# Optimization experiments

Hardware: AMD Instinct MI355X
Metric: run time of the kernel (lower is better)

The kernel has to match this reference:

```python
import jax, jax.numpy as jnp
import numpy as np
from jax import lax

B, S, T = 32, 24, 48           # batch, max_num_strokes, max_stroke_len
ENC, SCH, STH = 512, 512, 512  # enc_dim, scene_hdim, stroke_hdim


def _w(k, shape):
    return (jax.random.normal(k, shape, jnp.float32) / np.sqrt(shape[-1])).astype(jnp.float32)


def setup_inputs() -> dict:
    key = jax.random.key(0)
    ks = jax.random.split(key, 12)
    return {
        "enc_features": jax.random.normal(ks[0], (B, ENC), jnp.float32),
        "vector_sketch": jax.random.normal(ks[1], (B, S, T, 5), jnp.float32),
        # force max length == T and num strokes == S so torch's dynamic .max()
        # bounds coincide with the static shapes used here
        "batch_num_strokes": jnp.full((B, 1), S, jnp.int32),
        "batch_stroke_len": jax.random.randint(ks[2], (B, S), 1, T + 1, jnp.int32).at[0, 0].set(T),
        # scene LSTMCell (input = enc_dim + stroke_hdim), torch gate order i,f,g,o
        "W_sc_ih": _w(ks[3], (4 * SCH, ENC + STH)),
        "W_sc_hh": _w(ks[4], (4 * SCH, SCH)),
        "b_sc": jnp.zeros((4 * SCH,), jnp.float32),  # b_ih + b_hh folded
        # stroke LSTM layer 0 (input = scene_hdim + 5)
        "W0_ih": _w(ks[5], (4 * STH, SCH + 5)),
        "W0_hh": _w(ks[6], (4 * STH, STH)),
        "b0": jnp.zeros((4 * STH,), jnp.float32),
        # stroke LSTM layer 1 (input = stroke_hdim)
        "W1_ih": _w(ks[7], (4 * STH, STH)),
        "W1_hh": _w(ks[8], (4 * STH, STH)),
        "b1": jnp.zeros((4 * STH,), jnp.float32),
        # linear_output: stroke_hdim -> 5
        "W_out": _w(ks[9], (5, STH)),
        "b_out": jnp.zeros((5,), jnp.float32),
    }


def _lstm_cell(x, h, c, Wih, Whh, b):
    g = x @ Wih.T + h @ Whh.T + b
    i, f, gg, o = jnp.split(g, 4, axis=-1)
    c = jax.nn.sigmoid(f) * c + jax.nn.sigmoid(i) * jnp.tanh(gg)
    return jax.nn.sigmoid(o) * jnp.tanh(c), c


def _forward(enc_features, vector_sketch, W_sc_ih, W_sc_hh, b_sc, W0_ih, W0_hh, b0,
             W1_ih, W1_hh, b1, W_out, b_out, batch_stroke_len):
    nb = enc_features.shape[0]
    zs = jnp.zeros((nb, SCH), jnp.float32)
    init_tok0 = jnp.tile(jnp.array([[0., 0., 1., 0., 0.]], jnp.float32), (nb, 1))
    t_idx = jnp.arange(T + 1)

    def stroke_step(carry, xs):
        scene_h, scene_c, prev_tok, init_tok = carry
        sketch_s, lens_s = xs                       # (B,T,5), (B,)
        ctx = jnp.concatenate([enc_features, prev_tok], axis=-1)
        scene_h2, scene_c2 = _lstm_cell(ctx, scene_h, scene_c, W_sc_ih, W_sc_hh, b_sc)
        coords = jnp.concatenate([init_tok[:, None, :], sketch_s], axis=1)  # (B,T+1,5)
        lengths = lens_s + 1                        # pack lengths

        def time_step(c2, xt):
            h0, c0, h1, c1 = c2
            x_t, t = xt
            m = (t < lengths)[:, None]              # packed-sequence validity mask
            h0n, c0n = _lstm_cell(jnp.concatenate([scene_h2, x_t], axis=-1), h0, c0, W0_ih, W0_hh, b0)
            h1n, c1n = _lstm_cell(h0n, h1, c1, W1_ih, W1_hh, b1)
            h0 = jnp.where(m, h0n, h0); c0 = jnp.where(m, c0n, c0)
            h1 = jnp.where(m, h1n, h1); c1 = jnp.where(m, c1n, c1)
            return (h0, c0, h1, c1), jnp.where(m, h1, 0.0)  # pad_packed zero-pads outputs

        z = jnp.zeros((nb, STH), jnp.float32)
        (_, _, h1f, _), outs = lax.scan(time_step, (z, z, z, z), (jnp.swapaxes(coords, 0, 1), t_idx))
        # linear applied AFTER zero-padding, so padded-but-within-L steps get the bias (matches torch)
        out_coords = jnp.swapaxes(outs, 0, 1) @ W_out.T + b_out      # (B,T+1,5)
        L = jnp.max(lens_s)
        valid = (jnp.arange(T) < L)[None, :, None]
        stroke_out = jnp.where(valid, out_coords[:, :T, :], 0.0)     # (B,T,5)
        prev_tok = lax.stop_gradient(h1f)          # .detach() in torch
        last = jnp.clip(lens_s - 1, 0, None)
        init_tok2 = jnp.take_along_axis(sketch_s, last[:, None, None], axis=1)[:, 0, :]
        return (scene_h2, scene_c2, prev_tok, init_tok2), stroke_out

    xs = (jnp.swapaxes(vector_sketch, 0, 1), batch_stroke_len.T)     # (S,B,T,5), (S,B)
    _, outs = lax.scan(stroke_step, (zs, zs, zs, init_tok0), xs)
    return jnp.transpose(outs, (1, 0, 2, 3))       # (B,S,T,5)


def reference(enc_features, vector_sketch, batch_num_strokes, batch_stroke_len,
              W_sc_ih, W_sc_hh, b_sc, W0_ih, W0_hh, b0, W1_ih, W1_hh, b1, W_out, b_out):
    # batch_num_strokes only sets the (static) stroke loop bound S
    del batch_num_strokes
    return _forward(enc_features, vector_sketch, W_sc_ih, W_sc_hh, b_sc, W0_ih, W0_hh,
                    b0, W1_ih, W1_hh, b1, W_out, b_out, batch_stroke_len)
```

## Files before the change

kernel.cpp:

```cpp
#include <hip/hip_runtime.h>

#define NB 256
#define NT 256
#define AGT __HIP_MEMORY_SCOPE_AGENT
typedef unsigned long long ull;
typedef _Float16 f16;
typedef __attribute__((ext_vector_type(8))) _Float16 f16x8;
typedef __attribute__((ext_vector_type(4))) float f32x4;


#define BSTR 1056

struct __align__(16) SMem {
  unsigned short Bt[2][2][4 * 528];
  float X[2][4][8];
  int sLens[2][4];
  int sLmax[2];
};

__device__ __forceinline__ float sigm(float x) { return 1.0f / (1.0f + expf(-x)); }
__device__ __forceinline__ unsigned short f16b(float x) {
  union { _Float16 h; unsigned short u; } q; q.h = (_Float16)x; return q.u;
}
__device__ __forceinline__ ull pk4(float a, float b, float c, float d) {
  union { _Float16 h; unsigned short u; } q;
  ull r; q.h = (_Float16)a; r = q.u; q.h = (_Float16)b; r |= (ull)q.u << 16;
  q.h = (_Float16)c; r |= (ull)q.u << 32; q.h = (_Float16)d; r |= (ull)q.u << 48;
  return r;
}
__device__ __forceinline__ ull lda8(const ull* p) {
  return __hip_atomic_load(p, __ATOMIC_RELAXED, AGT);
}

extern "C" __global__ void __launch_bounds__(NT, 1)
rnn_decoder_kernel(const float* __restrict__ enc, const float* __restrict__ sketch,
                   const int* __restrict__ slen,
                   const float* __restrict__ Wsc_ih, const float* __restrict__ Wsc_hh,
                   const float* __restrict__ bsc,
                   const float* __restrict__ W0ih, const float* __restrict__ W0hh,
                   const float* __restrict__ b0,
                   const float* __restrict__ W1ih, const float* __restrict__ W1hh,
                   const float* __restrict__ b1,
                   const float* __restrict__ Wout, const float* __restrict__ bout,
                   float* __restrict__ out, float* __restrict__ ws)
{
  extern __shared__ char smraw[];
  SMem* sm = (SMem*)smraw;
  const int tid = threadIdx.x;
  const int w = blockIdx.x;
  const int team = w >> 5, slot = w & 31;
  const int lane = tid & 63;
  const int wq = tid >> 6;
  const int l15 = lane & 15;
  const int kq = lane >> 4;
  const int my_b = l15 & 3;
  const int my_u = wq * 4 + kq;

  ull* tb = (ull*)ws + (size_t)team * 6144;
  ull* h0T = tb;
  ull* h1T = tb + 2048;
  ull* sHg = tb + 4096;

  auto grow = [&](int r) { return ((r & 3) << 9) + slot * 16 + (r >> 2); };

  auto ldsB = [&](const unsigned short* Bp, int st) -> f16x8 {
    return *(const f16x8*)((const char*)Bp + my_b * BSTR + st * 64 + kq * 16);
  };
  auto mfma_gv = [&](const float* W, int stride, int coloff, const unsigned short* Bp, f32x4& acc) {
    const float* rp = W + (size_t)grow(wq * 16 + l15) * stride + coloff;
#pragma unroll
    for (int st = 0; st < 16; ++st) {
      const float* q = rp + st * 32 + kq * 8;
      float4 u0 = *(const float4*)q, u1 = *(const float4*)(q + 4);
      f16x8 a;
      a[0] = (f16)u0.x; a[1] = (f16)u0.y; a[2] = (f16)u0.z; a[3] = (f16)u0.w;
      a[4] = (f16)u1.x; a[5] = (f16)u1.y; a[6] = (f16)u1.z; a[7] = (f16)u1.w;
      acc = __builtin_amdgcn_mfma_f32_16x16x32_f16(a, ldsB(Bp, st), acc, 0, 0, 0);
    }
  };
  auto mfma_gs = [&](const float* W, const unsigned short* Bp, f32x4& acc) {
    const float* rp = W + (size_t)grow(wq * 16 + l15) * 517;
#pragma unroll
    for (int st = 0; st < 16; ++st) {
      const float* q = rp + st * 32 + kq * 8;
      f16x8 a;
#pragma unroll
      for (int j = 0; j < 8; ++j) a[j] = (f16)q[j];
      acc = __builtin_amdgcn_mfma_f32_16x16x32_f16(a, ldsB(Bp, st), acc, 0, 0, 0);
    }
  };

  auto stage4 = [&](const ull* s0, unsigned e0, unsigned short* Bp) {
    const ull* pA = s0 + 2 * tid;
    const ull* pB = pA + 1;
    const ull* pC = s0 + 512 + 2 * tid;
    const ull* pD = pC + 1;
    ull a = lda8(pA), b = lda8(pB), c = lda8(pC), d = lda8(pD);
    int spins = 0;
    while ((((unsigned)(a >> 32) ^ e0) | ((unsigned)(b >> 32) ^ e0) |
            ((unsigned)(c >> 32) ^ e0) | ((unsigned)(d >> 32) ^ e0)) != 0) {
      if (++spins > 40000) break;
      if (spins > 16) __builtin_amdgcn_s_sleep(1);
      if ((unsigned)(a >> 32) != e0) a = lda8(pA);
      if ((unsigned)(b >> 32) != e0) b = lda8(pB);
      if ((unsigned)(c >> 32) != e0) c = lda8(pC);
      if ((unsigned)(d >> 32) != e0) d = lda8(pD);
    }
    {
      int bb2 = tid >> 7, up = (2 * tid) & 255;
      *(ull*)((char*)Bp + bb2 * BSTR + up * 4) =
          (ull)(unsigned)a | ((ull)(unsigned)b << 32);
      int t2 = tid + 256;
      int bb3 = t2 >> 7, up2 = (2 * t2) & 255;
      *(ull*)((char*)Bp + bb3 * BSTR + up2 * 4) =
          (ull)(unsigned)c | ((ull)(unsigned)d << 32);
    }
  };

  f16x8 w0hh[16], w1ih[16], whh[16];
  {
    const float* r0 = W0hh + (size_t)grow(wq * 16 + l15) * 512;
    const float* r1 = W1ih + (size_t)grow(wq * 16 + l15) * 512;
    const float* r2 = W1hh + (size_t)grow(wq * 16 + l15) * 512;
#pragma unroll
    for (int st = 0; st < 16; ++st) {
      const int o = st * 32 + kq * 8;
      float4 u0, u1;
      f16x8 a;
      u0 = *(const float4*)(r0 + o); u1 = *(const float4*)(r0 + o + 4);
      a[0] = (f16)u0.x; a[1] = (f16)u0.y; a[2] = (f16)u0.z; a[3] = (f16)u0.w;
      a[4] = (f16)u1.x; a[5] = (f16)u1.y; a[6] = (f16)u1.z; a[7] = (f16)u1.w;
      w0hh[st] = a;
      u0 = *(const float4*)(r1 + o); u1 = *(const float4*)(r1 + o + 4);
      a[0] = (f16)u0.x; a[1] = (f16)u0.y; a[2] = (f16)u0.z; a[3] = (f16)u0.w;
      a[4] = (f16)u1.x; a[5] = (f16)u1.y; a[6] = (f16)u1.z; a[7] = (f16)u1.w;
      w1ih[st] = a;
      u0 = *(const float4*)(r2 + o); u1 = *(const float4*)(r2 + o + 4);
      a[0] = (f16)u0.x; a[1] = (f16)u0.y; a[2] = (f16)u0.z; a[3] = (f16)u0.w;
      a[4] = (f16)u1.x; a[5] = (f16)u1.y; a[6] = (f16)u1.z; a[7] = (f16)u1.w;
      whh[st] = a;
    }
  }
  float cb0[4], cb1[4], cbsc[4], cwx[4][5];
  {
    int gu = slot * 16 + my_u;
#pragma unroll
    for (int gi = 0; gi < 4; ++gi) {
      int gr = gi * 512 + gu;
      cb0[gi] = b0[gr]; cb1[gi] = b1[gr]; cbsc[gi] = bsc[gr];
#pragma unroll
      for (int j = 0; j < 5; ++j) cwx[gi][j] = W0ih[(size_t)gr * 517 + 512 + j];
    }
  }
  const int b_o = slot / 5, o_o = slot % 5;
  const bool oslot = (slot < 20);
  float wo[8]; float bo_r = 0.f;
  if (oslot && tid < 64) {
    bo_r = bout[o_o];
#pragma unroll
    for (int j = 0; j < 8; ++j) wo[j] = Wout[o_o * 512 + lane * 8 + j];
  }

  f32x4 e0reg = {0.f, 0.f, 0.f, 0.f};
  {
    int b2 = tid >> 6, c8 = tid & 63;
    const float* q = enc + (size_t)(4 * team + b2) * 512 + c8 * 8;
    float4 u0 = *(const float4*)q, u1 = *(const float4*)(q + 4);
    unsigned short* Bp = &sm->Bt[0][0][0];
    *(ull*)((char*)Bp + b2 * BSTR + c8 * 16) = pk4(u0.x, u0.y, u0.z, u0.w);
    *(ull*)((char*)Bp + b2 * BSTR + c8 * 16 + 8) = pk4(u1.x, u1.y, u1.z, u1.w);
    __syncthreads();
    mfma_gv(Wsc_ih, 1024, 0, Bp, e0reg);
  }

  float o_csc = 0.f, o_c0 = 0.f, o_h0 = 0.f, o_c1 = 0.f, o_h1 = 0.f;
  int pp = 0;

  for (int s = 0; s < 24; ++s) {
    const unsigned base = 51u * (unsigned)s;

    pp ^= 1;
    {
      int lv = (tid < 32) ? slen[tid * 24 + s] : 0;
      if (tid < 64) {
#pragma unroll
        for (int o2 = 1; o2 < 64; o2 <<= 1) lv = max(lv, __shfl_xor(lv, o2, 64));
        if (tid == 0) sm->sLmax[s & 1] = lv;
      }
      if (tid < 4) sm->sLens[s & 1][tid] = slen[(4 * team + tid) * 24 + s];
    }
    {
      unsigned short* Bp0 = &sm->Bt[pp][0][0];
      unsigned short* Bp1 = &sm->Bt[pp][1][0];
      if (s > 0) {
        stage4(h1T, base, Bp0);
        stage4(sHg + ((s - 1) & 1) * 1024, base - 50u, Bp1);
      }
      __syncthreads();
      f32x4 asc = {0.f, 0.f, 0.f, 0.f};
      if (s > 0) {
        mfma_gv(Wsc_ih, 1024, 512, Bp0, asc);
        mfma_gv(Wsc_hh, 512, 0, Bp1, asc);
      }
      float g[4];
#pragma unroll
      for (int gi = 0; gi < 4; ++gi) g[gi] = e0reg[gi] + cbsc[gi] + asc[gi];
      float c = sigm(g[1]) * o_csc + sigm(g[0]) * tanhf(g[2]);
      float h = sigm(g[3]) * tanhf(c);
      o_csc = c;
      o_c0 = o_h0 = o_c1 = o_h1 = 0.f;
      float hhi = __shfl_down(h, 16, 64);
      if (((kq & 1) == 0) && (l15 < 4)) {
        int chunk = my_b * 256 + slot * 8 + wq * 2 + (kq >> 1);
        unsigned pay = (unsigned)f16b(h) | ((unsigned)f16b(hhi) << 16);
        __hip_atomic_store(&sHg[(s & 1) * 1024 + chunk],
                           (ull)pay | ((ull)(base + 1u) << 32), __ATOMIC_RELAXED, AGT);
      }
    }

    pp ^= 1;
    f32x4 s0reg = {0.f, 0.f, 0.f, 0.f};
    {
      unsigned short* Bp0 = &sm->Bt[pp][0][0];
      if (tid < 4) {
        float xv[5];
        if (s == 0) { xv[0] = 0.f; xv[1] = 0.f; xv[2] = 1.f; xv[3] = 0.f; xv[4] = 0.f; }
        else {
          int bgl = 4 * team + tid;
          int lp = slen[bgl * 24 + (s - 1)];
          int last = min(max(lp - 1, 0), 47);
          const float* q = sketch + ((bgl * 24 + (s - 1)) * 48 + last) * 5;
#pragma unroll
          for (int j = 0; j < 5; ++j) xv[j] = q[j];
        }
#pragma unroll
        for (int j = 0; j < 5; ++j) sm->X[pp][tid][j] = xv[j];
      }
      stage4(sHg + (s & 1) * 1024, base + 1u, Bp0);
      __syncthreads();
      mfma_gs(W0ih, Bp0, s0reg);
      float g[4];
#pragma unroll
      for (int gi = 0; gi < 4; ++gi) {
        float xd = 0.f;
#pragma unroll
        for (int j = 0; j < 5; ++j) xd += cwx[gi][j] * sm->X[pp][my_b][j];
        g[gi] = s0reg[gi] + cb0[gi] + xd;
      }
      float c = sigm(g[1]) * o_c0 + sigm(g[0]) * tanhf(g[2]);
      o_c0 = c; o_h0 = sigm(g[3]) * tanhf(c);
      float hhi = __shfl_down(o_h0, 16, 64);
      if (((kq & 1) == 0) && (l15 < 4)) {
        int chunk = my_b * 256 + slot * 8 + wq * 2 + (kq >> 1);
        unsigned pay = (unsigned)f16b(o_h0) | ((unsigned)f16b(hhi) << 16);
        __hip_atomic_store(&h0T[chunk],
                           (ull)pay | ((ull)(base + 2u) << 32), __ATOMIC_RELAXED, AGT);
      }
    }

    for (int k = 0; k <= 48; ++k) {
      const bool doL0 = (k < 48), doPrev = (k > 0);
      const unsigned eSeq = base + 2u + (unsigned)k, sSeq = eSeq + 1u;
      pp ^= 1;
      unsigned short* B0p = &sm->Bt[pp][0][0];
      unsigned short* B1p = &sm->Bt[pp][1][0];
      if (doL0 && tid < 4) {
        const float* q = sketch + (((4 * team + tid) * 24 + s) * 48 + k) * 5;
#pragma unroll
        for (int j = 0; j < 5; ++j) sm->X[pp][tid][j] = q[j];
      }
      stage4(h0T + (k & 1) * 1024, eSeq, B0p);
      __syncthreads();

      f32x4 a0 = {0.f, 0.f, 0.f, 0.f}, a1 = {0.f, 0.f, 0.f, 0.f};
#pragma unroll
      for (int st = 0; st < 16; ++st) {
        f16x8 bb = ldsB(B0p, st);
        if (doL0) a0 = __builtin_amdgcn_mfma_f32_16x16x32_f16(w0hh[st], bb, a0, 0, 0, 0);
        a1 = __builtin_amdgcn_mfma_f32_16x16x32_f16(w1ih[st], bb, a1, 0, 0, 0);
      }
      const int Lb = sm->sLens[s & 1][my_b];
      if (doL0) {
        if ((k + 1) <= Lb) {
          float g[4];
#pragma unroll
          for (int gi = 0; gi < 4; ++gi) {
            float xd = 0.f;
#pragma unroll
            for (int j = 0; j < 5; ++j) xd += cwx[gi][j] * sm->X[pp][my_b][j];
            g[gi] = a0[gi] + s0reg[gi] + cb0[gi] + xd;
          }
          float c = sigm(g[1]) * o_c0 + sigm(g[0]) * tanhf(g[2]);
          o_c0 = c; o_h0 = sigm(g[3]) * tanhf(c);
        }
        float hhi0 = __shfl_down(o_h0, 16, 64);
        if (((kq & 1) == 0) && (l15 < 4)) {
          int chunk = my_b * 256 + slot * 8 + wq * 2 + (kq >> 1);
          unsigned p0 = (unsigned)f16b(o_h0) | ((unsigned)f16b(hhi0) << 16);
          __hip_atomic_store(&h0T[((k + 1) & 1) * 1024 + chunk],
                             (ull)p0 | ((ull)sSeq << 32), __ATOMIC_RELAXED, AGT);
        }
      }
      if (doPrev) {
        stage4(h1T + ((k - 1) & 1) * 1024, eSeq, B1p);
        __syncthreads();
#pragma unroll
        for (int st = 0; st < 16; ++st)
          a1 = __builtin_amdgcn_mfma_f32_16x16x32_f16(whh[st], ldsB(B1p, st), a1, 0, 0, 0);
      }
      if (k <= Lb) {
        float g[4];
#pragma unroll
        for (int gi = 0; gi < 4; ++gi) g[gi] = a1[gi] + cb1[gi];
        float c = sigm(g[1]) * o_c1 + sigm(g[0]) * tanhf(g[2]);
        o_c1 = c; o_h1 = sigm(g[3]) * tanhf(c);
      }
      float hhi1 = __shfl_down(o_h1, 16, 64);
      if (((kq & 1) == 0) && (l15 < 4)) {
        int chunk = my_b * 256 + slot * 8 + wq * 2 + (kq >> 1);
        unsigned p1 = (unsigned)f16b(o_h1) | ((unsigned)f16b(hhi1) << 16);
        __hip_atomic_store(&h1T[(k & 1) * 1024 + chunk],
                           (ull)p1 | ((ull)sSeq << 32), __ATOMIC_RELAXED, AGT);
      }

      if (doPrev && oslot && tid < 64) {
        f16x8 hv = *(const f16x8*)((const char*)B1p + b_o * BSTR + lane * 16);
        float sd = 0.f;
#pragma unroll
        for (int j = 0; j < 8; ++j) sd += (float)hv[j] * wo[j];
#pragma unroll
        for (int o2 = 1; o2 < 64; o2 <<= 1) sd += __shfl_xor(sd, o2, 64);
        if (tid == 0) {
          int tt = k - 1;
          float val = 0.f;
          if (tt < sm->sLmax[s & 1])
            val = (tt > sm->sLens[s & 1][b_o]) ? bo_r : (sd + bo_r);
          out[(((4 * team + b_o) * 24 + s) * 48 + tt) * 5 + o_o] = val;
        }
      }
    }
  }
}

extern "C" void kernel_launch(void* const* d_in, const int* in_sizes, int n_in,
                              void* d_out, int out_size, void* d_ws, size_t ws_size,
                              hipStream_t stream) {
  (void)in_sizes; (void)n_in; (void)out_size; (void)ws_size;
  int lds_bytes = 98304;
  hipFuncSetAttribute((const void*)rnn_decoder_kernel,
                      hipFuncAttributeMaxDynamicSharedMemorySize, lds_bytes);
  hipMemsetAsync(d_ws, 0, 8 * 6144 * 8, stream);
  rnn_decoder_kernel<<<dim3(NB), dim3(NT), lds_bytes, stream>>>(
      (const float*)d_in[0],
      (const float*)d_in[1],
      (const int*)d_in[3],
      (const float*)d_in[4],
      (const float*)d_in[5],
      (const float*)d_in[6],
      (const float*)d_in[7],
      (const float*)d_in[8],
      (const float*)d_in[9],
      (const float*)d_in[10],
      (const float*)d_in[11],
      (const float*)d_in[12],
      (const float*)d_in[13],
      (const float*)d_in[14],
      (float*)d_out, (float*)d_ws);
}
```

Before: 4.057 ms.

## Stage recurrent hidden states per-wave to remove block barriers in time loop

Inside the 48-step inner recurrence, each wave now polls and stages the full h0/h1 vectors into its own private LDS buffer, using batched inline-asm cache-bypassing loads. This removes the two __syncthreads per step. The stroke's sketch inputs are preloaded into LDS once per stroke instead of once per step, and the output projection is spread across waves. The cost is redundant global polling traffic, four times the LDS staging work, and reliance on inline asm with sc0 sc1 for coherent reads.

```diff
diff --git a/kernel.cpp b/kernel.cpp
--- a/kernel.cpp
+++ b/kernel.cpp
@@ -7,13 +7,16 @@
 typedef _Float16 f16;
 typedef __attribute__((ext_vector_type(8))) _Float16 f16x8;
 typedef __attribute__((ext_vector_type(4))) float f32x4;
+typedef __attribute__((ext_vector_type(4))) unsigned u32x4;
 
 
 #define BSTR 1056
 
 struct __align__(16) SMem {
-  unsigned short Bt[2][2][4 * 528];
-  float X[2][4][8];
+  unsigned short Wv[4][2][4 * 528];
+  unsigned short Bs[2][4 * 528];
+  float Xs[48][4][8];
+  float X0[4][8];
   int sLens[2][4];
   int sLmax[2];
 };
@@ -30,6 +33,22 @@
 }
 __device__ __forceinline__ ull lda8(const ull* p) {
   return __hip_atomic_load(p, __ATOMIC_RELAXED, AGT);
+}
+__device__ __forceinline__ u32x4 ld1x16(const void* p) {
+  u32x4 r;
+  asm volatile("global_load_dwordx4 %0, %1, off sc0 sc1\ns_waitcnt vmcnt(0)"
+               : "=&v"(r) : "v"(p) : "memory");
+  return r;
+}
+__device__ __forceinline__ void issue4(const void* p0, const void* p1,
+                                       const void* p2, const void* p3,
+                                       u32x4& a, u32x4& b, u32x4& c, u32x4& d) {
+  asm volatile("global_load_dwordx4 %0, %4, off sc0 sc1\n"
+               "global_load_dwordx4 %1, %5, off sc0 sc1\n"
+               "global_load_dwordx4 %2, %6, off sc0 sc1\n"
+               "global_load_dwordx4 %3, %7, off sc0 sc1"
+               : "=&v"(a), "=&v"(b), "=&v"(c), "=&v"(d)
+               : "v"(p0), "v"(p1), "v"(p2), "v"(p3) : "memory");
 }
 
 extern "C" __global__ void __launch_bounds__(NT, 1)
@@ -117,6 +136,43 @@
     }
   };
 
+  auto stageW = [&](const ull* s0, unsigned e0, unsigned short* Wt) {
+    const char* p = (const char*)(s0 + 16 * lane);
+    u32x4 v0, v1, v2, v3, v4, v5, v6, v7;
+    issue4(p, p + 16, p + 32, p + 48, v0, v1, v2, v3);
+    issue4(p + 64, p + 80, p + 96, p + 112, v4, v5, v6, v7);
+    asm volatile("s_waitcnt vmcnt(0)"
+                 : "+v"(v0), "+v"(v1), "+v"(v2), "+v"(v3),
+                   "+v"(v4), "+v"(v5), "+v"(v6), "+v"(v7) :: "memory");
+    int spins = 0;
+    for (;;) {
+      unsigned bad = (v0.y ^ e0) | (v0.w ^ e0) | (v1.y ^ e0) | (v1.w ^ e0) |
+                     (v2.y ^ e0) | (v2.w ^ e0) | (v3.y ^ e0) | (v3.w ^ e0) |
+                     (v4.y ^ e0) | (v4.w ^ e0) | (v5.y ^ e0) | (v5.w ^ e0) |
+                     (v6.y ^ e0) | (v6.w ^ e0) | (v7.y ^ e0) | (v7.w ^ e0);
+      if (!bad) break;
+      if (++spins > 40000) break;
+      if (spins > 16) __builtin_amdgcn_s_sleep(1);
+      if ((v0.y ^ e0) | (v0.w ^ e0)) v0 = ld1x16(p);
+      if ((v1.y ^ e0) | (v1.w ^ e0)) v1 = ld1x16(p + 16);
+      if ((v2.y ^ e0) | (v2.w ^ e0)) v2 = ld1x16(p + 32);
+      if ((v3.y ^ e0) | (v3.w ^ e0)) v3 = ld1x16(p + 48);
+      if ((v4.y ^ e0) | (v4.w ^ e0)) v4 = ld1x16(p + 64);
+      if ((v5.y ^ e0) | (v5.w ^ e0)) v5 = ld1x16(p + 80);
+      if ((v6.y ^ e0) | (v6.w ^ e0)) v6 = ld1x16(p + 96);
+      if ((v7.y ^ e0) | (v7.w ^ e0)) v7 = ld1x16(p + 112);
+    }
+    char* d = (char*)Wt + (lane >> 4) * BSTR + 64 * l15;
+    *(ull*)(d)      = (ull)v0.x | ((ull)v0.z << 32);
+    *(ull*)(d + 8)  = (ull)v1.x | ((ull)v1.z << 32);
+    *(ull*)(d + 16) = (ull)v2.x | ((ull)v2.z << 32);
+    *(ull*)(d + 24) = (ull)v3.x | ((ull)v3.z << 32);
+    *(ull*)(d + 32) = (ull)v4.x | ((ull)v4.z << 32);
+    *(ull*)(d + 40) = (ull)v5.x | ((ull)v5.z << 32);
+    *(ull*)(d + 48) = (ull)v6.x | ((ull)v6.z << 32);
+    *(ull*)(d + 56) = (ull)v7.x | ((ull)v7.z << 32);
+  };
+
   f16x8 w0hh[16], w1ih[16], whh[16];
   {
     const float* r0 = W0hh + (size_t)grow(wq * 16 + l15) * 512;
@@ -154,8 +210,9 @@
   }
   const int b_o = slot / 5, o_o = slot % 5;
   const bool oslot = (slot < 20);
+  const int owave = slot & 3;
   float wo[8]; float bo_r = 0.f;
-  if (oslot && tid < 64) {
+  if (oslot) {
     bo_r = bout[o_o];
 #pragma unroll
     for (int j = 0; j < 8; ++j) wo[j] = Wout[o_o * 512 + lane * 8 + j];
@@ -166,7 +223,7 @@
     int b2 = tid >> 6, c8 = tid & 63;
     const float* q = enc + (size_t)(4 * team + b2) * 512 + c8 * 8;
     float4 u0 = *(const float4*)q, u1 = *(const float4*)(q + 4);
-    unsigned short* Bp = &sm->Bt[0][0][0];
+    unsigned short* Bp = &sm->Bs[0][0];
     *(ull*)((char*)Bp + b2 * BSTR + c8 * 16) = pk4(u0.x, u0.y, u0.z, u0.w);
     *(ull*)((char*)Bp + b2 * BSTR + c8 * 16 + 8) = pk4(u1.x, u1.y, u1.z, u1.w);
     __syncthreads();
@@ -174,12 +231,12 @@
   }
 
   float o_csc = 0.f, o_c0 = 0.f, o_h0 = 0.f, o_c1 = 0.f, o_h1 = 0.f;
-  int pp = 0;
+  unsigned short* myB0 = &sm->Wv[wq][0][0];
+  unsigned short* myB1 = &sm->Wv[wq][1][0];
 
   for (int s = 0; s < 24; ++s) {
     const unsigned base = 51u * (unsigned)s;
 
-    pp ^= 1;
     {
       int lv = (tid < 32) ? slen[tid * 24 + s] : 0;
       if (tid < 64) {
@@ -190,8 +247,8 @@
       if (tid < 4) sm->sLens[s & 1][tid] = slen[(4 * team + tid) * 24 + s];
     }
     {
-      unsigned short* Bp0 = &sm->Bt[pp][0][0];
-      unsigned short* Bp1 = &sm->Bt[pp][1][0];
+      unsigned short* Bp0 = &sm->Bs[0][0];
+      unsigned short* Bp1 = &sm->Bs[1][0];
       if (s > 0) {
         stage4(h1T, base, Bp0);
         stage4(sHg + ((s - 1) & 1) * 1024, base - 50u, Bp1);
@@ -218,10 +275,10 @@
       }
     }
 
-    pp ^= 1;
     f32x4 s0reg = {0.f, 0.f, 0.f, 0.f};
     {
-      unsigned short* Bp0 = &sm->Bt[pp][0][0];
+      __syncthreads();
+      unsigned short* Bp0 = &sm->Bs[0][0];
       if (tid < 4) {
         float xv[5];
         if (s == 0) { xv[0] = 0.f; xv[1] = 0.f; xv[2] = 1.f; xv[3] = 0.f; xv[4] = 0.f; }
@@ -234,7 +291,12 @@
           for (int j = 0; j < 5; ++j) xv[j] = q[j];
         }
 #pragma unroll
-        for (int j = 0; j < 5; ++j) sm->X[pp][tid][j] = xv[j];
+        for (int j = 0; j < 5; ++j) sm->X0[tid][j] = xv[j];
+      }
+      for (int e = tid; e < 960; e += NT) {
+        int k2 = e / 20, r2 = e % 20, b2 = r2 / 5, j2 = r2 % 5;
+        sm->Xs[k2][b2][j2] =
+            sketch[(((4 * team + b2) * 24 + s) * 48 + k2) * 5 + j2];
       }
       stage4(sHg + (s & 1) * 1024, base + 1u, Bp0);
       __syncthreads();
@@ -244,7 +306,7 @@
       for (int gi = 0; gi < 4; ++gi) {
         float xd = 0.f;
 #pragma unroll
-        for (int j = 0; j < 5; ++j) xd += cwx[gi][j] * sm->X[pp][my_b][j];
+        for (int j = 0; j < 5; ++j) xd += cwx[gi][j] * sm->X0[my_b][j];
         g[gi] = s0reg[gi] + cb0[gi] + xd;
       }
       float c = sigm(g[1]) * o_c0 + sigm(g[0]) * tanhf(g[2]);
@@ -258,36 +320,27 @@
       }
     }
 
+    const int Lb = sm->sLens[s & 1][my_b];
+    const int Lmax_s = sm->sLmax[s & 1];
+    const int Lb_o = sm->sLens[s & 1][oslot ? b_o : 0];
+
     for (int k = 0; k <= 48; ++k) {
       const bool doL0 = (k < 48), doPrev = (k > 0);
       const unsigned eSeq = base + 2u + (unsigned)k, sSeq = eSeq + 1u;
-      pp ^= 1;
-      unsigned short* B0p = &sm->Bt[pp][0][0];
-      unsigned short* B1p = &sm->Bt[pp][1][0];
-      if (doL0 && tid < 4) {
-        const float* q = sketch + (((4 * team + tid) * 24 + s) * 48 + k) * 5;
-#pragma unroll
-        for (int j = 0; j < 5; ++j) sm->X[pp][tid][j] = q[j];
-      }
-      stage4(h0T + (k & 1) * 1024, eSeq, B0p);
-      __syncthreads();
-
+
+      stageW(h0T + (k & 1) * 1024, eSeq, myB0);
       f32x4 a0 = {0.f, 0.f, 0.f, 0.f}, a1 = {0.f, 0.f, 0.f, 0.f};
-#pragma unroll
-      for (int st = 0; st < 16; ++st) {
-        f16x8 bb = ldsB(B0p, st);
-        if (doL0) a0 = __builtin_amdgcn_mfma_f32_16x16x32_f16(w0hh[st], bb, a0, 0, 0, 0);
-        a1 = __builtin_amdgcn_mfma_f32_16x16x32_f16(w1ih[st], bb, a1, 0, 0, 0);
-      }
-      const int Lb = sm->sLens[s & 1][my_b];
       if (doL0) {
+#pragma unroll
+        for (int st = 0; st < 16; ++st)
+          a0 = __builtin_amdgcn_mfma_f32_16x16x32_f16(w0hh[st], ldsB(myB0, st), a0, 0, 0, 0);
         if ((k + 1) <= Lb) {
           float g[4];
 #pragma unroll
           for (int gi = 0; gi < 4; ++gi) {
             float xd = 0.f;
 #pragma unroll
-            for (int j = 0; j < 5; ++j) xd += cwx[gi][j] * sm->X[pp][my_b][j];
+            for (int j = 0; j < 5; ++j) xd += cwx[gi][j] * sm->Xs[k][my_b][j];
             g[gi] = a0[gi] + s0reg[gi] + cb0[gi] + xd;
           }
           float c = sigm(g[1]) * o_c0 + sigm(g[0]) * tanhf(g[2]);
@@ -300,13 +353,17 @@
           __hip_atomic_store(&h0T[((k + 1) & 1) * 1024 + chunk],
                              (ull)p0 | ((ull)sSeq << 32), __ATOMIC_RELAXED, AGT);
         }
-      }
+        asm volatile("" ::: "memory");
+      }
+#pragma unroll
+      for (int st = 0; st < 16; ++st)
+        a1 = __builtin_amdgcn_mfma_f32_16x16x32_f16(w1ih[st], ldsB(myB0, st), a1, 0, 0, 0);
+
       if (doPrev) {
-        stage4(h1T + ((k - 1) & 1) * 1024, eSeq, B1p);
-        __syncthreads();
+        stageW(h1T + ((k - 1) & 1) * 1024, eSeq, myB1);
 #pragma unroll
         for (int st = 0; st < 16; ++st)
-          a1 = __builtin_amdgcn_mfma_f32_16x16x32_f16(whh[st], ldsB(B1p, st), a1, 0, 0, 0);
+          a1 = __builtin_amdgcn_mfma_f32_16x16x32_f16(whh[st], ldsB(myB1, st), a1, 0, 0, 0);
       }
       if (k <= Lb) {
         float g[4];
@@ -322,19 +379,19 @@
         __hip_atomic_store(&h1T[(k & 1) * 1024 + chunk],
                            (ull)p1 | ((ull)sSeq << 32), __ATOMIC_RELAXED, AGT);
       }
-
-      if (doPrev && oslot && tid < 64) {
-        f16x8 hv = *(const f16x8*)((const char*)B1p + b_o * BSTR + lane * 16);
+      asm volatile("" ::: "memory");
+
+      if (doPrev && oslot && wq == owave) {
+        f16x8 hv = *(const f16x8*)((const char*)myB1 + b_o * BSTR + lane * 16);
         float sd = 0.f;
 #pragma unroll
         for (int j = 0; j < 8; ++j) sd += (float)hv[j] * wo[j];
 #pragma unroll
         for (int o2 = 1; o2 < 64; o2 <<= 1) sd += __shfl_xor(sd, o2, 64);
-        if (tid == 0) {
+        if (lane == 0) {
           int tt = k - 1;
           float val = 0.f;
-          if (tt < sm->sLmax[s & 1])
-            val = (tt > sm->sLens[s & 1][b_o]) ? bo_r : (sd + bo_r);
+          if (tt < Lmax_s) val = (tt > Lb_o) ? bo_r : (sd + bo_r);
           out[(((4 * team + b_o) * 24 + s) * 48 + tt) * 5 + o_o] = val;
         }
       }
```

After: 8.125 ms. 100% more time.

## Split block waves into layer-0 and layer-1 groups with LDS flag handoff

Applied to the files above, without the earlier changes.

Each block's four waves are specialised: two waves run the layer-0 stroke LSTM recurrence and two run layer 1, each wave handling two gate tiles, instead of all waves doing both layers in lockstep. Workgroup-scoped LDS flags replace __syncthreads inside the time loop so layer 0 can run ahead on step k+1 while layer 1 finishes step k. h0 gets a 4-deep ring buffer and the per-stroke sketch inputs are preloaded into LDS. Register pressure rises from holding 32-fragment weight arrays per wave, and the flag-based spin synchronisation is more fragile than barriers.

```diff
diff --git a/kernel.cpp b/kernel.cpp
--- a/kernel.cpp
+++ b/kernel.cpp
@@ -3,6 +3,7 @@
 #define NB 256
 #define NT 256
 #define AGT __HIP_MEMORY_SCOPE_AGENT
+#define WGS __HIP_MEMORY_SCOPE_WORKGROUP
 typedef unsigned long long ull;
 typedef _Float16 f16;
 typedef __attribute__((ext_vector_type(8))) _Float16 f16x8;
@@ -12,10 +13,17 @@
 #define BSTR 1056
 
 struct __align__(16) SMem {
-  unsigned short Bt[2][2][4 * 528];
-  float X[2][4][8];
+  unsigned short T0[2][4 * 528];
+  unsigned short T1[2][4 * 528];
+  unsigned short Bs[2][4 * 528];
+  float Xs[48][4][8];
+  float X0[4][8];
+  float sS0[16][4][4];
+  float sC0[16][4];
+  float sH0[16][4];
   int sLens[2][4];
   int sLmax[2];
+  unsigned gFlag[8];
 };
 
 __device__ __forceinline__ float sigm(float x) { return 1.0f / (1.0f + expf(-x)); }
@@ -55,28 +63,31 @@
   const int kq = lane >> 4;
   const int my_b = l15 & 3;
   const int my_u = wq * 4 + kq;
-
-  ull* tb = (ull*)ws + (size_t)team * 6144;
+  const int wid2 = wq & 1;
+  const int uA = 8 * wid2 + kq, uB = uA + 4;
+
+  ull* tb = (ull*)ws + (size_t)team * 8192;
   ull* h0T = tb;
-  ull* h1T = tb + 2048;
-  ull* sHg = tb + 4096;
+  ull* h1T = tb + 4096;
+  ull* sHg = tb + 6144;
 
   auto grow = [&](int r) { return ((r & 3) << 9) + slot * 16 + (r >> 2); };
-
   auto ldsB = [&](const unsigned short* Bp, int st) -> f16x8 {
     return *(const f16x8*)((const char*)Bp + my_b * BSTR + st * 64 + kq * 16);
   };
+  auto mkfrag = [&](const float* q) -> f16x8 {
+    float4 u0 = *(const float4*)q, u1 = *(const float4*)(q + 4);
+    f16x8 a;
+    a[0]=(f16)u0.x; a[1]=(f16)u0.y; a[2]=(f16)u0.z; a[3]=(f16)u0.w;
+    a[4]=(f16)u1.x; a[5]=(f16)u1.y; a[6]=(f16)u1.z; a[7]=(f16)u1.w;
+    return a;
+  };
   auto mfma_gv = [&](const float* W, int stride, int coloff, const unsigned short* Bp, f32x4& acc) {
     const float* rp = W + (size_t)grow(wq * 16 + l15) * stride + coloff;
 #pragma unroll
-    for (int st = 0; st < 16; ++st) {
-      const float* q = rp + st * 32 + kq * 8;
-      float4 u0 = *(const float4*)q, u1 = *(const float4*)(q + 4);
-      f16x8 a;
-      a[0] = (f16)u0.x; a[1] = (f16)u0.y; a[2] = (f16)u0.z; a[3] = (f16)u0.w;
-      a[4] = (f16)u1.x; a[5] = (f16)u1.y; a[6] = (f16)u1.z; a[7] = (f16)u1.w;
-      acc = __builtin_amdgcn_mfma_f32_16x16x32_f16(a, ldsB(Bp, st), acc, 0, 0, 0);
-    }
+    for (int st = 0; st < 16; ++st)
+      acc = __builtin_amdgcn_mfma_f32_16x16x32_f16(mkfrag(rp + st * 32 + kq * 8),
+                                                   ldsB(Bp, st), acc, 0, 0, 0);
   };
   auto mfma_gs = [&](const float* W, const unsigned short* Bp, f32x4& acc) {
     const float* rp = W + (size_t)grow(wq * 16 + l15) * 517;
@@ -99,63 +110,98 @@
     int spins = 0;
     while ((((unsigned)(a >> 32) ^ e0) | ((unsigned)(b >> 32) ^ e0) |
             ((unsigned)(c >> 32) ^ e0) | ((unsigned)(d >> 32) ^ e0)) != 0) {
-      if (++spins > 40000) break;
+      if (++spins > 60000) break;
       if (spins > 16) __builtin_amdgcn_s_sleep(1);
       if ((unsigned)(a >> 32) != e0) a = lda8(pA);
       if ((unsigned)(b >> 32) != e0) b = lda8(pB);
       if ((unsigned)(c >> 32) != e0) c = lda8(pC);
       if ((unsigned)(d >> 32) != e0) d = lda8(pD);
     }
-    {
-      int bb2 = tid >> 7, up = (2 * tid) & 255;
-      *(ull*)((char*)Bp + bb2 * BSTR + up * 4) =
-          (ull)(unsigned)a | ((ull)(unsigned)b << 32);
-      int t2 = tid + 256;
-      int bb3 = t2 >> 7, up2 = (2 * t2) & 255;
-      *(ull*)((char*)Bp + bb3 * BSTR + up2 * 4) =
-          (ull)(unsigned)c | ((ull)(unsigned)d << 32);
-    }
-  };
-
-  f16x8 w0hh[16], w1ih[16], whh[16];
+    int bb2 = tid >> 7, up = (2 * tid) & 255;
+    *(ull*)((char*)Bp + bb2 * BSTR + up * 4) = (ull)(unsigned)a | ((ull)(unsigned)b << 32);
+    int t2 = tid + 256, bb3 = t2 >> 7, up2 = (2 * t2) & 255;
+    *(ull*)((char*)Bp + bb3 * BSTR + up2 * 4) = (ull)(unsigned)c | ((ull)(unsigned)d << 32);
+  };
+
+  auto stageH = [&](const ull* src, unsigned e0, unsigned short* T) {
+    const ull* p = src + wid2 * 512 + lane;
+    ull v[8];
+#pragma unroll
+    for (int i = 0; i < 8; ++i) v[i] = lda8(p + 64 * i);
+    int spins = 0;
+    for (;;) {
+      unsigned bad = 0;
+#pragma unroll
+      for (int i = 0; i < 8; ++i) bad |= ((unsigned)(v[i] >> 32)) ^ e0;
+      if (!bad) break;
+      if (++spins > 60000) break;
+      if (spins > 8) __builtin_amdgcn_s_sleep(1);
+#pragma unroll
+      for (int i = 0; i < 8; ++i)
+        if ((unsigned)(v[i] >> 32) != e0) v[i] = lda8(p + 64 * i);
+    }
+#pragma unroll
+    for (int i = 0; i < 8; ++i) {
+      int c = wid2 * 512 + lane + 64 * i;
+      *(unsigned*)((char*)T + (c >> 8) * BSTR + (c & 255) * 4) = (unsigned)v[i];
+    }
+  };
+  auto fstore = [&](int idx, unsigned v) {
+    __hip_atomic_store(&sm->gFlag[idx], v, __ATOMIC_RELEASE, WGS);
+  };
+  auto fwait = [&](int idx, unsigned v) {
+    int spins = 0;
+    while (__hip_atomic_load(&sm->gFlag[idx], __ATOMIC_ACQUIRE, WGS) < v) {
+      if (++spins > 200000) break;
+      if (spins > 8) __builtin_amdgcn_s_sleep(1);
+    }
+  };
+
+  if (tid < 8) sm->gFlag[tid] = 0u;
+
+  f16x8 wA[32], wB[32];
   {
-    const float* r0 = W0hh + (size_t)grow(wq * 16 + l15) * 512;
-    const float* r1 = W1ih + (size_t)grow(wq * 16 + l15) * 512;
-    const float* r2 = W1hh + (size_t)grow(wq * 16 + l15) * 512;
-#pragma unroll
-    for (int st = 0; st < 16; ++st) {
-      const int o = st * 32 + kq * 8;
-      float4 u0, u1;
-      f16x8 a;
-      u0 = *(const float4*)(r0 + o); u1 = *(const float4*)(r0 + o + 4);
-      a[0] = (f16)u0.x; a[1] = (f16)u0.y; a[2] = (f16)u0.z; a[3] = (f16)u0.w;
-      a[4] = (f16)u1.x; a[5] = (f16)u1.y; a[6] = (f16)u1.z; a[7] = (f16)u1.w;
-      w0hh[st] = a;
-      u0 = *(const float4*)(r1 + o); u1 = *(const float4*)(r1 + o + 4);
-      a[0] = (f16)u0.x; a[1] = (f16)u0.y; a[2] = (f16)u0.z; a[3] = (f16)u0.w;
-      a[4] = (f16)u1.x; a[5] = (f16)u1.y; a[6] = (f16)u1.z; a[7] = (f16)u1.w;
-      w1ih[st] = a;
-      u0 = *(const float4*)(r2 + o); u1 = *(const float4*)(r2 + o + 4);
-      a[0] = (f16)u0.x; a[1] = (f16)u0.y; a[2] = (f16)u0.z; a[3] = (f16)u0.w;
-      a[4] = (f16)u1.x; a[5] = (f16)u1.y; a[6] = (f16)u1.z; a[7] = (f16)u1.w;
-      whh[st] = a;
+    const float* SA = (wq < 2) ? W0hh : W1ih;
+#pragma unroll
+    for (int t2 = 0; t2 < 2; ++t2) {
+      const float* rp = SA + (size_t)grow(32 * wid2 + 16 * t2 + l15) * 512;
+#pragma unroll
+      for (int st = 0; st < 16; ++st) wA[t2 * 16 + st] = mkfrag(rp + st * 32 + kq * 8);
+    }
+    if (wq >= 2) {
+#pragma unroll
+      for (int t2 = 0; t2 < 2; ++t2) {
+        const float* rp = W1hh + (size_t)grow(32 * wid2 + 16 * t2 + l15) * 512;
+#pragma unroll
+        for (int st = 0; st < 16; ++st) wB[t2 * 16 + st] = mkfrag(rp + st * 32 + kq * 8);
+      }
     }
   }
-  float cb0[4], cb1[4], cbsc[4], cwx[4][5];
-  {
-    int gu = slot * 16 + my_u;
+  const int guA = slot * 16 + uA, guB = slot * 16 + uB;
+  float cbA[4], cbB[4], cwA[4][5], cwB[4][5];
+  if (wq < 2) {
 #pragma unroll
     for (int gi = 0; gi < 4; ++gi) {
-      int gr = gi * 512 + gu;
-      cb0[gi] = b0[gr]; cb1[gi] = b1[gr]; cbsc[gi] = bsc[gr];
-#pragma unroll
-      for (int j = 0; j < 5; ++j) cwx[gi][j] = W0ih[(size_t)gr * 517 + 512 + j];
+      cbA[gi] = b0[gi * 512 + guA]; cbB[gi] = b0[gi * 512 + guB];
+#pragma unroll
+      for (int j = 0; j < 5; ++j) {
+        cwA[gi][j] = W0ih[(size_t)(gi * 512 + guA) * 517 + 512 + j];
+        cwB[gi][j] = W0ih[(size_t)(gi * 512 + guB) * 517 + 512 + j];
+      }
+    }
+  } else {
+#pragma unroll
+    for (int gi = 0; gi < 4; ++gi) {
+      cbA[gi] = b1[gi * 512 + guA]; cbB[gi] = b1[gi * 512 + guB];
     }
   }
+  float cbsc[4];
+#pragma unroll
+  for (int gi = 0; gi < 4; ++gi) cbsc[gi] = bsc[gi * 512 + slot * 16 + my_u];
   const int b_o = slot / 5, o_o = slot % 5;
   const bool oslot = (slot < 20);
   float wo[8]; float bo_r = 0.f;
-  if (oslot && tid < 64) {
+  if (oslot) {
     bo_r = bout[o_o];
 #pragma unroll
     for (int j = 0; j < 8; ++j) wo[j] = Wout[o_o * 512 + lane * 8 + j];
@@ -166,20 +212,18 @@
     int b2 = tid >> 6, c8 = tid & 63;
     const float* q = enc + (size_t)(4 * team + b2) * 512 + c8 * 8;
     float4 u0 = *(const float4*)q, u1 = *(const float4*)(q + 4);
-    unsigned short* Bp = &sm->Bt[0][0][0];
+    unsigned short* Bp = &sm->Bs[0][0];
     *(ull*)((char*)Bp + b2 * BSTR + c8 * 16) = pk4(u0.x, u0.y, u0.z, u0.w);
     *(ull*)((char*)Bp + b2 * BSTR + c8 * 16 + 8) = pk4(u1.x, u1.y, u1.z, u1.w);
     __syncthreads();
     mfma_gv(Wsc_ih, 1024, 0, Bp, e0reg);
   }
 
-  float o_csc = 0.f, o_c0 = 0.f, o_h0 = 0.f, o_c1 = 0.f, o_h1 = 0.f;
-  int pp = 0;
+  float o_csc = 0.f;
 
   for (int s = 0; s < 24; ++s) {
     const unsigned base = 51u * (unsigned)s;
 
-    pp ^= 1;
     {
       int lv = (tid < 32) ? slen[tid * 24 + s] : 0;
       if (tid < 64) {
@@ -190,8 +234,8 @@
       if (tid < 4) sm->sLens[s & 1][tid] = slen[(4 * team + tid) * 24 + s];
     }
     {
-      unsigned short* Bp0 = &sm->Bt[pp][0][0];
-      unsigned short* Bp1 = &sm->Bt[pp][1][0];
+      unsigned short* Bp0 = &sm->Bs[0][0];
+      unsigned short* Bp1 = &sm->Bs[1][0];
       if (s > 0) {
         stage4(h1T, base, Bp0);
         stage4(sHg + ((s - 1) & 1) * 1024, base - 50u, Bp1);
@@ -208,23 +252,21 @@
       float c = sigm(g[1]) * o_csc + sigm(g[0]) * tanhf(g[2]);
       float h = sigm(g[3]) * tanhf(c);
       o_csc = c;
-      o_c0 = o_h0 = o_c1 = o_h1 = 0.f;
       float hhi = __shfl_down(h, 16, 64);
       if (((kq & 1) == 0) && (l15 < 4)) {
         int chunk = my_b * 256 + slot * 8 + wq * 2 + (kq >> 1);
-        unsigned pay = (unsigned)f16b(h) | ((unsigned)f16b(hhi) << 16);
         __hip_atomic_store(&sHg[(s & 1) * 1024 + chunk],
-                           (ull)pay | ((ull)(base + 1u) << 32), __ATOMIC_RELAXED, AGT);
-      }
-    }
-
-    pp ^= 1;
-    f32x4 s0reg = {0.f, 0.f, 0.f, 0.f};
+                           (ull)((unsigned)f16b(h) | ((unsigned)f16b(hhi) << 16)) |
+                           ((ull)(base + 1u) << 32), __ATOMIC_RELAXED, AGT);
+      }
+    }
+
     {
-      unsigned short* Bp0 = &sm->Bt[pp][0][0];
+      __syncthreads();
+      unsigned short* Bp0 = &sm->Bs[0][0];
       if (tid < 4) {
         float xv[5];
-        if (s == 0) { xv[0] = 0.f; xv[1] = 0.f; xv[2] = 1.f; xv[3] = 0.f; xv[4] = 0.f; }
+        if (s == 0) { xv[0]=0.f; xv[1]=0.f; xv[2]=1.f; xv[3]=0.f; xv[4]=0.f; }
         else {
           int bgl = 4 * team + tid;
           int lp = slen[bgl * 24 + (s - 1)];
@@ -234,111 +276,187 @@
           for (int j = 0; j < 5; ++j) xv[j] = q[j];
         }
 #pragma unroll
-        for (int j = 0; j < 5; ++j) sm->X[pp][tid][j] = xv[j];
+        for (int j = 0; j < 5; ++j) sm->X0[tid][j] = xv[j];
+      }
+      for (int e = tid; e < 960; e += NT) {
+        int k2 = e / 20, r2 = e % 20, b2 = r2 / 5, j2 = r2 % 5;
+        sm->Xs[k2][b2][j2] = sketch[(((4 * team + b2) * 24 + s) * 48 + k2) * 5 + j2];
       }
       stage4(sHg + (s & 1) * 1024, base + 1u, Bp0);
       __syncthreads();
+      f32x4 s0reg = {0.f, 0.f, 0.f, 0.f};
       mfma_gs(W0ih, Bp0, s0reg);
+      float tb0[4], twx[4][5];
+#pragma unroll
+      for (int gi = 0; gi < 4; ++gi) {
+        int gr = gi * 512 + slot * 16 + my_u;
+        tb0[gi] = b0[gr];
+#pragma unroll
+        for (int j = 0; j < 5; ++j) twx[gi][j] = W0ih[(size_t)gr * 517 + 512 + j];
+      }
       float g[4];
 #pragma unroll
       for (int gi = 0; gi < 4; ++gi) {
         float xd = 0.f;
 #pragma unroll
-        for (int j = 0; j < 5; ++j) xd += cwx[gi][j] * sm->X[pp][my_b][j];
-        g[gi] = s0reg[gi] + cb0[gi] + xd;
-      }
-      float c = sigm(g[1]) * o_c0 + sigm(g[0]) * tanhf(g[2]);
-      o_c0 = c; o_h0 = sigm(g[3]) * tanhf(c);
-      float hhi = __shfl_down(o_h0, 16, 64);
+        for (int j = 0; j < 5; ++j) xd += twx[gi][j] * sm->X0[my_b][j];
+        g[gi] = s0reg[gi] + tb0[gi] + xd;
+      }
+      float c = sigm(g[1]) * 0.f + sigm(g[0]) * tanhf(g[2]);
+      float h = sigm(g[3]) * tanhf(c);
+      if (l15 < 4) {
+        sm->sC0[my_u][my_b] = c;
+        sm->sH0[my_u][my_b] = h;
+        sm->sS0[my_u][my_b][0] = s0reg[0]; sm->sS0[my_u][my_b][1] = s0reg[1];
+        sm->sS0[my_u][my_b][2] = s0reg[2]; sm->sS0[my_u][my_b][3] = s0reg[3];
+      }
+      float hhi = __shfl_down(h, 16, 64);
       if (((kq & 1) == 0) && (l15 < 4)) {
         int chunk = my_b * 256 + slot * 8 + wq * 2 + (kq >> 1);
-        unsigned pay = (unsigned)f16b(o_h0) | ((unsigned)f16b(hhi) << 16);
         __hip_atomic_store(&h0T[chunk],
-                           (ull)pay | ((ull)(base + 2u) << 32), __ATOMIC_RELAXED, AGT);
-      }
-    }
-
-    for (int k = 0; k <= 48; ++k) {
-      const bool doL0 = (k < 48), doPrev = (k > 0);
-      const unsigned eSeq = base + 2u + (unsigned)k, sSeq = eSeq + 1u;
-      pp ^= 1;
-      unsigned short* B0p = &sm->Bt[pp][0][0];
-      unsigned short* B1p = &sm->Bt[pp][1][0];
-      if (doL0 && tid < 4) {
-        const float* q = sketch + (((4 * team + tid) * 24 + s) * 48 + k) * 5;
-#pragma unroll
-        for (int j = 0; j < 5; ++j) sm->X[pp][tid][j] = q[j];
-      }
-      stage4(h0T + (k & 1) * 1024, eSeq, B0p);
+                           (ull)((unsigned)f16b(h) | ((unsigned)f16b(hhi) << 16)) |
+                           ((ull)(base + 2u) << 32), __ATOMIC_RELAXED, AGT);
+      }
       __syncthreads();
-
-      f32x4 a0 = {0.f, 0.f, 0.f, 0.f}, a1 = {0.f, 0.f, 0.f, 0.f};
-#pragma unroll
-      for (int st = 0; st < 16; ++st) {
-        f16x8 bb = ldsB(B0p, st);
-        if (doL0) a0 = __builtin_amdgcn_mfma_f32_16x16x32_f16(w0hh[st], bb, a0, 0, 0, 0);
-        a1 = __builtin_amdgcn_mfma_f32_16x16x32_f16(w1ih[st], bb, a1, 0, 0, 0);
-      }
-      const int Lb = sm->sLens[s & 1][my_b];
-      if (doL0) {
-        if ((k + 1) <= Lb) {
-          float g[4];
-#pragma unroll
-          for (int gi = 0; gi < 4; ++gi) {
-            float xd = 0.f;
-#pragma unroll
-            for (int j = 0; j < 5; ++j) xd += cwx[gi][j] * sm->X[pp][my_b][j];
-            g[gi] = a0[gi] + s0reg[gi] + cb0[gi] + xd;
+    }
+
+    const int Lb = sm->sLens[s & 1][my_b];
+
+    if (wq < 2) {
+      float cA = sm->sC0[uA][my_b], hA = sm->sH0[uA][my_b];
+      float cB = sm->sC0[uB][my_b], hB = sm->sH0[uB][my_b];
+      float s0A0 = sm->sS0[uA][my_b][0], s0A1 = sm->sS0[uA][my_b][1],
+            s0A2 = sm->sS0[uA][my_b][2], s0A3 = sm->sS0[uA][my_b][3];
+      float s0B0 = sm->sS0[uB][my_b][0], s0B1 = sm->sS0[uB][my_b][1],
+            s0B2 = sm->sS0[uB][my_b][2], s0B3 = sm->sS0[uB][my_b][3];
+      for (int k = 0; k <= 48; ++k) {
+        const unsigned eSeq = base + 2u + (unsigned)k, sSeq = eSeq + 1u;
+        if (k >= 2) { fwait(4, base + (unsigned)k); fwait(5, base + (unsigned)k); }
+        stageH(h0T + (size_t)(k & 3) * 1024, eSeq, sm->T0[k & 1]);
+        asm volatile("s_waitcnt lgkmcnt(0)" ::: "memory");
+        fstore(wid2, eSeq);
+        fwait(wid2 ^ 1, eSeq);
+        __builtin_amdgcn_sched_barrier(0);
+        if (k < 48) {
+          f32x4 aA = {0.f,0.f,0.f,0.f}, aB = {0.f,0.f,0.f,0.f};
+#pragma unroll
+          for (int st = 0; st < 16; ++st) {
+            f16x8 bb = ldsB(sm->T0[k & 1], st);
+            aA = __builtin_amdgcn_mfma_f32_16x16x32_f16(wA[st], bb, aA, 0, 0, 0);
+            aB = __builtin_amdgcn_mfma_f32_16x16x32_f16(wA[16 + st], bb, aB, 0, 0, 0);
           }
-          float c = sigm(g[1]) * o_c0 + sigm(g[0]) * tanhf(g[2]);
-          o_c0 = c; o_h0 = sigm(g[3]) * tanhf(c);
-        }
-        float hhi0 = __shfl_down(o_h0, 16, 64);
+          if ((k + 1) <= Lb) {
+            float xd[4];
+#pragma unroll
+            for (int gi = 0; gi < 4; ++gi) {
+              xd[gi] = 0.f;
+#pragma unroll
+              for (int j = 0; j < 5; ++j) xd[gi] += cwA[gi][j] * sm->Xs[k][my_b][j];
+            }
+            float g0 = aA[0] + s0A0 + cbA[0] + xd[0];
+            float g1 = aA[1] + s0A1 + cbA[1] + xd[1];
+            float g2 = aA[2] + s0A2 + cbA[2] + xd[2];
+            float g3 = aA[3] + s0A3 + cbA[3] + xd[3];
+            cA = sigm(g1) * cA + sigm(g0) * tanhf(g2);
+            hA = sigm(g3) * tanhf(cA);
+#pragma unroll
+            for (int gi = 0; gi < 4; ++gi) {
+              xd[gi] = 0.f;
+#pragma unroll
+              for (int j = 0; j < 5; ++j) xd[gi] += cwB[gi][j] * sm->Xs[k][my_b][j];
+            }
+            g0 = aB[0] + s0B0 + cbB[0] + xd[0];
+            g1 = aB[1] + s0B1 + cbB[1] + xd[1];
+            g2 = aB[2] + s0B2 + cbB[2] + xd[2];
+            g3 = aB[3] + s0B3 + cbB[3] + xd[3];
+            cB = sigm(g1) * cB + sigm(g0) * tanhf(g2);
+            hB = sigm(g3) * tanhf(cB);
+          }
+          float hA2 = __shfl_down(hA, 16, 64);
+          float hB2 = __shfl_down(hB, 16, 64);
+          if (((kq & 1) == 0) && (l15 < 4)) {
+            int cbase = my_b * 256 + slot * 8 + 4 * wid2 + (kq >> 1);
+            size_t pb = (size_t)((k + 1) & 3) * 1024;
+            __hip_atomic_store(&h0T[pb + cbase],
+                               (ull)((unsigned)f16b(hA) | ((unsigned)f16b(hA2) << 16)) |
+                               ((ull)sSeq << 32), __ATOMIC_RELAXED, AGT);
+            __hip_atomic_store(&h0T[pb + cbase + 2],
+                               (ull)((unsigned)f16b(hB) | ((unsigned)f16b(hB2) << 16)) |
+                               ((ull)sSeq << 32), __ATOMIC_RELAXED, AGT);
+          }
+        }
+      }
+    } else {
+      const int Lmax_s = sm->sLmax[s & 1];
+      const int Lb_o = sm->sLens[s & 1][oslot ? b_o : 0];
+      float cA = 0.f, hA = 0.f, cB = 0.f, hB = 0.f;
+      for (int k = 0; k <= 48; ++k) {
+        const unsigned eSeq = base + 2u + (unsigned)k, sSeq = eSeq + 1u;
+        const bool doPrev = (k > 0);
+        if (doPrev) {
+          stageH(h1T + (size_t)((k - 1) & 1) * 1024, eSeq, sm->T1[k & 1]);
+          asm volatile("s_waitcnt lgkmcnt(0)" ::: "memory");
+          fstore(2 + wid2, eSeq);
+        }
+        fwait(0, eSeq); fwait(1, eSeq);
+        __builtin_amdgcn_sched_barrier(0);
+        f32x4 aA = {0.f,0.f,0.f,0.f}, aB = {0.f,0.f,0.f,0.f};
+#pragma unroll
+        for (int st = 0; st < 16; ++st) {
+          f16x8 bb = ldsB(sm->T0[k & 1], st);
+          aA = __builtin_amdgcn_mfma_f32_16x16x32_f16(wA[st], bb, aA, 0, 0, 0);
+          aB = __builtin_amdgcn_mfma_f32_16x16x32_f16(wA[16 + st], bb, aB, 0, 0, 0);
+        }
+        fstore(4 + wid2, eSeq);
+        if (doPrev) {
+          fwait(2 + (wid2 ^ 1), eSeq);
+          __builtin_amdgcn_sched_barrier(0);
+#pragma unroll
+          for (int st = 0; st < 16; ++st) {
+            f16x8 bb = ldsB(sm->T1[k & 1], st);
+            aA = __builtin_amdgcn_mfma_f32_16x16x32_f16(wB[st], bb, aA, 0, 0, 0);
+            aB = __builtin_amdgcn_mfma_f32_16x16x32_f16(wB[16 + st], bb, aB, 0, 0, 0);
+          }
+        }
+        if (k <= Lb) {
+          float g0 = aA[0] + cbA[0], g1 = aA[1] + cbA[1],
+                g2 = aA[2] + cbA[2], g3 = aA[3] + cbA[3];
+          cA = sigm(g1) * cA + sigm(g0) * tanhf(g2);
+          hA = sigm(g3) * tanhf(cA);
+          g0 = aB[0] + cbB[0]; g1 = aB[1] + cbB[1];
+          g2 = aB[2] + cbB[2]; g3 = aB[3] + cbB[3];
+          cB = sigm(g1) * cB + sigm(g0) * tanhf(g2);
+          hB = sigm(g3) * tanhf(cB);
+        }
+        float hA2 = __shfl_down(hA, 16, 64);
+        float hB2 = __shfl_down(hB, 16, 64);
         if (((kq & 1) == 0) && (l15 < 4)) {
-          int chunk = my_b * 256 + slot * 8 + wq * 2 + (kq >> 1);
-          unsigned p0 = (unsigned)f16b(o_h0) | ((unsigned)f16b(hhi0) << 16);
-          __hip_atomic_store(&h0T[((k + 1) & 1) * 1024 + chunk],
-                             (ull)p0 | ((ull)sSeq << 32), __ATOMIC_RELAXED, AGT);
-        }
-      }
-      if (doPrev) {
-        stage4(h1T + ((k - 1) & 1) * 1024, eSeq, B1p);
-        __syncthreads();
-#pragma unroll
-        for (int st = 0; st < 16; ++st)
-          a1 = __builtin_amdgcn_mfma_f32_16x16x32_f16(whh[st], ldsB(B1p, st), a1, 0, 0, 0);
-      }
-      if (k <= Lb) {
-        float g[4];
-#pragma unroll
-        for (int gi = 0; gi < 4; ++gi) g[gi] = a1[gi] + cb1[gi];
-        float c = sigm(g[1]) * o_c1 + sigm(g[0]) * tanhf(g[2]);
-        o_c1 = c; o_h1 = sigm(g[3]) * tanhf(c);
-      }
-      float hhi1 = __shfl_down(o_h1, 16, 64);
-      if (((kq & 1) == 0) && (l15 < 4)) {
-        int chunk = my_b * 256 + slot * 8 + wq * 2 + (kq >> 1);
-        unsigned p1 = (unsigned)f16b(o_h1) | ((unsigned)f16b(hhi1) << 16);
-        __hip_atomic_store(&h1T[(k & 1) * 1024 + chunk],
-                           (ull)p1 | ((ull)sSeq << 32), __ATOMIC_RELAXED, AGT);
-      }
-
-      if (doPrev && oslot && tid < 64) {
-        f16x8 hv = *(const f16x8*)((const char*)B1p + b_o * BSTR + lane * 16);
-        float sd = 0.f;
-#pragma unroll
-        for (int j = 0; j < 8; ++j) sd += (float)hv[j] * wo[j];
-#pragma unroll
-        for (int o2 = 1; o2 < 64; o2 <<= 1) sd += __shfl_xor(sd, o2, 64);
-        if (tid == 0) {
-          int tt = k - 1;
-          float val = 0.f;
-          if (tt < sm->sLmax[s & 1])
-            val = (tt > sm->sLens[s & 1][b_o]) ? bo_r : (sd + bo_r);
-          out[(((4 * team + b_o) * 24 + s) * 48 + tt) * 5 + o_o] = val;
-        }
-      }
-    }
+          int cbase = my_b * 256 + slot * 8 + 4 * wid2 + (kq >> 1);
+          size_t pb = (size_t)(k & 1) * 1024;
+          __hip_atomic_store(&h1T[pb + cbase],
+                             (ull)((unsigned)f16b(hA) | ((unsigned)f16b(hA2) << 16)) |
+                             ((ull)sSeq << 32), __ATOMIC_RELAXED, AGT);
+          __hip_atomic_store(&h1T[pb + cbase + 2],
+                             (ull)((unsigned)f16b(hB) | ((unsigned)f16b(hB2) << 16)) |
+                             ((ull)sSeq << 32), __ATOMIC_RELAXED, AGT);
+        }
+        if (doPrev && oslot && wq == 2) {
+          f16x8 hv = *(const f16x8*)((const char*)sm->T1[k & 1] + b_o * BSTR + lane * 16);
+          float sd = 0.f;
+#pragma unroll
+          for (int j = 0; j < 8; ++j) sd += (float)hv[j] * wo[j];
+#pragma unroll
+          for (int o2 = 1; o2 < 64; o2 <<= 1) sd += __shfl_xor(sd, o2, 64);
+          if (lane == 0) {
+            int tt = k - 1;
+            float val = 0.f;
+            if (tt < Lmax_s) val = (tt > Lb_o) ? bo_r : (sd + bo_r);
+            out[(((4 * team + b_o) * 24 + s) * 48 + tt) * 5 + o_o] = val;
+          }
+        }
+      }
+    }
+    __syncthreads();
   }
 }
 
@@ -349,7 +467,7 @@
   int lds_bytes = 98304;
   hipFuncSetAttribute((const void*)rnn_decoder_kernel,
                       hipFuncAttributeMaxDynamicSharedMemorySize, lds_bytes);
-  hipMemsetAsync(d_ws, 0, 8 * 6144 * 8, stream);
+  hipMemsetAsync(d_ws, 0, 524288, stream);
   rnn_decoder_kernel<<<dim3(NB), dim3(NT), lds_bytes, stream>>>(
       (const float*)d_in[0],
       (const float*)d_in[1],
```

Measured after the change: 5.851 ms. 44.2% more time.
